# Kernel tuning notes

Measured on AMD Instinct MI355X. Metric: run time of the kernel, lower is better.

Reference implementation:

```python
import jax, jax.numpy as jnp
import numpy as np
from jax import lax

B, T, H, E, N, K = 1024, 64, 512, 200000, 50000, 2
LN_EPS = 1e-5


def _layernorm(x, w, b):
    m = jnp.mean(x, axis=-1, keepdims=True)
    v = jnp.mean((x - m) ** 2, axis=-1, keepdims=True)
    return (x - m) * lax.rsqrt(v + LN_EPS) * w + b


def setup_inputs() -> dict:
    key = jax.random.key(0)
    ks = jax.random.split(key, 12)
    s = 1.0 / np.sqrt(H)
    actions = jax.random.randint(ks[0], (B, T), 0, E, dtype=jnp.int32)
    # each graph stops at a random step in [T//2, T]; actions after that are -1 (stop)
    stop_len = jax.random.randint(ks[1], (B,), T // 2, T + 1, dtype=jnp.int32)
    actions = jnp.where(jnp.arange(T)[None, :] >= stop_len[:, None], -1, actions)
    return {
        "actions_seq": actions,
        "edge_tokens": jax.random.normal(ks[2], (E, H), dtype=jnp.float32),
        "stop_indices": jnp.full((B,), E, dtype=jnp.int32),  # never equals a real edge id
        "question_tokens": jax.random.normal(ks[3], (B, H), dtype=jnp.float32),
        "node_tokens": jax.random.normal(ks[4], (N, H), dtype=jnp.float32),
        "start_node_locals": jax.random.randint(ks[5], (B * K,), 0, N, dtype=jnp.int32),
        "start_ptr": (jnp.arange(B + 1, dtype=jnp.int32) * K),
        "w_ih": jax.random.normal(ks[6], (3 * H, H), dtype=jnp.float32) * s,
        "w_hh": jax.random.normal(ks[7], (3 * H, H), dtype=jnp.float32) * s,
        "b_ih": jax.random.normal(ks[8], (3 * H,), dtype=jnp.float32) * s,
        "b_hh": jax.random.normal(ks[9], (3 * H,), dtype=jnp.float32) * s,
        "ln_w": jnp.ones((H,), dtype=jnp.float32),
        "ln_b": jnp.zeros((H,), dtype=jnp.float32),
    }


def reference(actions_seq, edge_tokens, stop_indices, question_tokens, node_tokens,
              start_node_locals, start_ptr, w_ih, w_hh, b_ih, b_hh, ln_w, ln_b):
    num_graphs, num_steps = actions_seq.shape
    max_edge = edge_tokens.shape[0]

    # start state: segment-mean of selected node tokens per graph
    counts = start_ptr[1:] - start_ptr[:-1]  # [B]
    seg = jnp.repeat(jnp.arange(num_graphs), counts,
                     total_repeat_length=start_node_locals.shape[0])
    start_sum = jax.ops.segment_sum(node_tokens[start_node_locals], seg,
                                    num_segments=num_graphs)  # [B,H]
    denom = jnp.maximum(counts, 1).astype(start_sum.dtype)[:, None]
    start_state = start_sum / denom

    h0 = _layernorm(question_tokens + start_state, ln_w, ln_b)
    done0 = jnp.zeros((num_graphs,), dtype=bool)

    def step(carry, a):  # a: [B] actions at this step
        h, done = carry
        emb = _layernorm(h, ln_w, ln_b)  # emitted BEFORE the update, as in torch
        is_stop = (a == stop_indices) | (a < 0)
        active = (~done) & (~is_stop)
        idx = jnp.clip(a, 0, max_edge - 1)
        x = edge_tokens[idx]  # [B,H] gather (dropout p=0 -> identity)
        gi = x @ w_ih.T + b_ih  # [B,3H]
        gh = h @ w_hh.T + b_hh  # [B,3H]
        i_r, i_z, i_n = jnp.split(gi, 3, axis=-1)
        h_r, h_z, h_n = jnp.split(gh, 3, axis=-1)
        r = jax.nn.sigmoid(i_r + h_r)
        z = jax.nn.sigmoid(i_z + h_z)
        n = jnp.tanh(i_n + r * h_n)
        h_next = (1.0 - z) * n + z * h
        h = jnp.where(active[:, None], h_next, h)
        done = done | is_stop
        return (h, done), emb

    (_, _), embs = lax.scan(step, (h0, done0), actions_seq.T)  # embs: [T,B,H]
    return jnp.transpose(embs, (1, 0, 2))  # [B,T,H]
```

## Files before the change

kernel.cpp:

```cpp
#include <hip/hip_runtime.h>
#include <math.h>

#define NB 1024
#define NT 64
#define NH 512
#define NE 200000
#define LN_EPS 1e-5f

typedef __bf16 bf16;
typedef __attribute__((ext_vector_type(8))) __bf16 bf16x8;
typedef __attribute__((ext_vector_type(4))) float f32x4;

__device__ __forceinline__ void ln_stats(float sum, float sq, float& mean, float& rstd) {
#pragma unroll
  for (int o = 32; o > 0; o >>= 1) {
    sum += __shfl_down(sum, o);
    sq  += __shfl_down(sq, o);
  }
  __shared__ float red[8];
  const int wid = threadIdx.x >> 6;
  if ((threadIdx.x & 63) == 0) { red[wid * 2] = sum; red[wid * 2 + 1] = sq; }
  __syncthreads();
  if (threadIdx.x == 0) {
    const float ts = red[0] + red[2] + red[4] + red[6];
    const float tq = red[1] + red[3] + red[5] + red[7];
    const float m  = ts * (1.0f / NH);
    const float var = tq * (1.0f / NH) - m * m;
    red[0] = m;
    red[1] = rsqrtf(var + LN_EPS);
  }
  __syncthreads();
  mean = red[0];
  rstd = red[1];
}

__device__ __forceinline__ float sigmoid_f(float x) {
  return 1.0f / (1.0f + __expf(-x));
}
__device__ __forceinline__ float tanh_f(float x) {
  x = fminf(fmaxf(x, -15.0f), 15.0f);
  const float e = __expf(2.0f * x);
  return (e - 1.0f) / (e + 1.0f);
}

__global__ void active_kernel(const int* __restrict__ actions,
                              const int* __restrict__ stopidx,
                              int* __restrict__ act_mask) {
  const int b = blockIdx.x * blockDim.x + threadIdx.x;
  if (b >= NB) return;
  const int si = stopidx[b];
  bool done = false;
  for (int t = 0; t < NT; ++t) {
    const int a = actions[b * NT + t];
    const bool is_stop = (a == si) || (a < 0);
    act_mask[b * NT + t] = (!done && !is_stop) ? 1 : 0;
    done = done || is_stop;
  }
}

__global__ void wcvt_kernel(const float* __restrict__ wih,
                            const float* __restrict__ whh,
                            bf16* __restrict__ wihb, bf16* __restrict__ whhb) {
  const int i = (blockIdx.x * 256 + threadIdx.x) * 4;
  const float4 a = *(const float4*)&wih[i];
  const float4 b = *(const float4*)&whh[i];
  union { bf16 h[4]; uint2 u; } pa, pb;
  pa.h[0] = (bf16)a.x; pa.h[1] = (bf16)a.y; pa.h[2] = (bf16)a.z; pa.h[3] = (bf16)a.w;
  pb.h[0] = (bf16)b.x; pb.h[1] = (bf16)b.y; pb.h[2] = (bf16)b.z; pb.h[3] = (bf16)b.w;
  *(uint2*)&wihb[i] = pa.u;
  *(uint2*)&whhb[i] = pb.u;
}

__global__ void xall_kernel(const int* __restrict__ actions,
                            const float* __restrict__ edges,
                            bf16* __restrict__ xbf) {
  const int row = blockIdx.x;
  int a = actions[row];
  a = min(max(a, 0), NE - 1);
  const int i = threadIdx.x * 2;
  const float2 v = *(const float2*)&edges[(size_t)a * NH + i];
  union { bf16 h[2]; unsigned u; } p;
  p.h[0] = (bf16)v.x; p.h[1] = (bf16)v.y;
  *(unsigned*)&xbf[(size_t)row * NH + i] = p.u;
}

__global__ void h0_kernel(const float* __restrict__ q,
                          const float* __restrict__ nodes,
                          const int* __restrict__ locals,
                          const int* __restrict__ ptr,
                          const float* __restrict__ lnw,
                          const float* __restrict__ lnb,
                          float* __restrict__ h0, bf16* __restrict__ h0b) {
  const int b = blockIdx.x;
  const int i = threadIdx.x * 2;
  const int p0 = ptr[b], p1 = ptr[b + 1];
  const float denom = fmaxf((float)(p1 - p0), 1.0f);
  float s0 = 0.f, s1 = 0.f;
  for (int p = p0; p < p1; ++p) {
    const int node = locals[p];
    const float2 nv = *(const float2*)&nodes[(size_t)node * NH + i];
    s0 += nv.x; s1 += nv.y;
  }
  const float2 qv = *(const float2*)&q[(size_t)b * NH + i];
  const float v0 = qv.x + s0 / denom;
  const float v1 = qv.y + s1 / denom;
  float mean, rstd;
  ln_stats(v0 + v1, v0 * v0 + v1 * v1, mean, rstd);
  const float2 lw = *(const float2*)&lnw[i];
  const float2 lb = *(const float2*)&lnb[i];
  float2 o;
  o.x = (v0 - mean) * rstd * lw.x + lb.x;
  o.y = (v1 - mean) * rstd * lw.y + lb.y;
  *(float2*)&h0[(size_t)b * NH + i] = o;
  union { bf16 h[2]; unsigned u; } p;
  p.h[0] = (bf16)o.x; p.h[1] = (bf16)o.y;
  *(unsigned*)&h0b[(size_t)b * NH + i] = p.u;
}

#define BK 128
__global__ __launch_bounds__(512) void gates_kernel(
    const float* __restrict__ hs_t, float* __restrict__ hs_n,
    const bf16* __restrict__ hbf, bf16* __restrict__ hbf_n,
    const bf16* __restrict__ xbf,
    const bf16* __restrict__ wihb, const bf16* __restrict__ whhb,
    const float* __restrict__ b_ih, const float* __restrict__ b_hh,
    const int* __restrict__ act_mask, int t) {
  __shared__ bf16 Xs[64][BK + 8];
  __shared__ bf16 Hs[64][BK + 8];
  __shared__ bf16 Wi[96][BK + 8];
  __shared__ bf16 Wh[96][BK + 8];
  __shared__ int s_any;

  const int tid = threadIdx.x;
  const int c0 = blockIdx.x * 32;
  const int b0 = blockIdx.y * 64;

  if (tid == 0) s_any = 0;
  __syncthreads();
  if (tid < 64 && act_mask[(b0 + tid) * NT + t]) s_any = 1;
  __syncthreads();

  if (!s_any) {
    const int row = tid >> 3, c4 = (tid & 7) * 4;
    const size_t off = (size_t)(b0 + row) * NH + c0 + c4;
    const float4 v = *(const float4*)&hs_t[off];
    *(float4*)&hs_n[off] = v;
    union { bf16 h[4]; uint2 u; } p;
    p.h[0] = (bf16)v.x; p.h[1] = (bf16)v.y; p.h[2] = (bf16)v.z; p.h[3] = (bf16)v.w;
    *(uint2*)&hbf_n[off] = p.u;
    return;
  }

  const int wave = tid >> 6, lane = tid & 63;
  const int ln15 = lane & 15, q8 = (lane >> 4) * 8;
  const int wrow = (wave & 3) * 16;
  const int nt = wave >> 2;

  f32x4 aR = {0, 0, 0, 0}, aZ = {0, 0, 0, 0}, aNI = {0, 0, 0, 0}, aNH = {0, 0, 0, 0};

  for (int kb = 0; kb < NH; kb += BK) {
    if (kb) __syncthreads();
#pragma unroll
    for (int i = 0; i < 2; ++i) {
      const int idx = tid + 512 * i;
      const int row = idx >> 4, c8 = (idx & 15) * 8;
      *(int4*)&Hs[row][c8] = *(const int4*)&hbf[(size_t)(b0 + row) * NH + kb + c8];
      *(int4*)&Xs[row][c8] =
          *(const int4*)&xbf[((size_t)(b0 + row) * NT + t) * NH + kb + c8];
    }
#pragma unroll
    for (int i = 0; i < 3; ++i) {
      const int idx = tid + 512 * i;
      const int row = idx >> 4, c8 = (idx & 15) * 8;
      const int g = row >> 5, n = row & 31;
      const size_t gr = ((size_t)g * NH + c0 + n) * NH + kb + c8;
      *(int4*)&Wi[row][c8] = *(const int4*)&wihb[gr];
      *(int4*)&Wh[row][c8] = *(const int4*)&whhb[gr];
    }
    __syncthreads();
#pragma unroll
    for (int k = 0; k < BK; k += 32) {
      const bf16x8 ax = *(const bf16x8*)&Xs[wrow + ln15][k + q8];
      const bf16x8 ah = *(const bf16x8*)&Hs[wrow + ln15][k + q8];
      const int wr = nt * 16 + ln15;
      const bf16x8 biR = *(const bf16x8*)&Wi[wr][k + q8];
      const bf16x8 bhR = *(const bf16x8*)&Wh[wr][k + q8];
      const bf16x8 biZ = *(const bf16x8*)&Wi[32 + wr][k + q8];
      const bf16x8 bhZ = *(const bf16x8*)&Wh[32 + wr][k + q8];
      const bf16x8 biN = *(const bf16x8*)&Wi[64 + wr][k + q8];
      const bf16x8 bhN = *(const bf16x8*)&Wh[64 + wr][k + q8];
      aR = __builtin_amdgcn_mfma_f32_16x16x32_bf16(ax, biR, aR, 0, 0, 0);
      aR = __builtin_amdgcn_mfma_f32_16x16x32_bf16(ah, bhR, aR, 0, 0, 0);
      aZ = __builtin_amdgcn_mfma_f32_16x16x32_bf16(ax, biZ, aZ, 0, 0, 0);
      aZ = __builtin_amdgcn_mfma_f32_16x16x32_bf16(ah, bhZ, aZ, 0, 0, 0);
      aNI = __builtin_amdgcn_mfma_f32_16x16x32_bf16(ax, biN, aNI, 0, 0, 0);
      aNH = __builtin_amdgcn_mfma_f32_16x16x32_bf16(ah, bhN, aNH, 0, 0, 0);
    }
  }

  const int c = c0 + nt * 16 + ln15;
  const float bR = b_ih[c] + b_hh[c];
  const float bZ = b_ih[NH + c] + b_hh[NH + c];
  const float bI = b_ih[2 * NH + c];
  const float bH = b_hh[2 * NH + c];
  const int mbase = b0 + wrow + (lane >> 4) * 4;
#pragma unroll
  for (int i = 0; i < 4; ++i) {
    const int m = mbase + i;
    const int act = act_mask[m * NT + t];
    const float hp = hs_t[(size_t)m * NH + c];
    const float r = sigmoid_f(aR[i] + bR);
    const float z = sigmoid_f(aZ[i] + bZ);
    const float n = tanh_f(aNI[i] + bI + r * (aNH[i] + bH));
    const float o = act ? ((1.0f - z) * n + z * hp) : hp;
    hs_n[(size_t)m * NH + c] = o;
    hbf_n[(size_t)m * NH + c] = (bf16)o;
  }
}

__global__ void ln_all_kernel(const float* __restrict__ hs,
                              const float* __restrict__ lnw,
                              const float* __restrict__ lnb,
                              float* __restrict__ out) {
  const int r = blockIdx.x;
  const int t = r >> 10, b = r & (NB - 1);
  const int i = threadIdx.x * 2;
  const float2 hv = *(const float2*)&hs[(size_t)r * NH + i];
  float mean, rstd;
  ln_stats(hv.x + hv.y, hv.x * hv.x + hv.y * hv.y, mean, rstd);
  const float2 lw = *(const float2*)&lnw[i];
  const float2 lb = *(const float2*)&lnb[i];
  float2 o;
  o.x = (hv.x - mean) * rstd * lw.x + lb.x;
  o.y = (hv.y - mean) * rstd * lw.y + lb.y;
  *(float2*)&out[((size_t)b * NT + t) * NH + i] = o;
}

extern "C" void kernel_launch(void* const* d_in, const int* in_sizes, int n_in,
                              void* d_out, int out_size, void* d_ws, size_t ws_size,
                              hipStream_t stream) {
  const int*   actions      = (const int*)d_in[0];
  const float* edge_tokens  = (const float*)d_in[1];
  const int*   stop_indices = (const int*)d_in[2];
  const float* question     = (const float*)d_in[3];
  const float* node_tokens  = (const float*)d_in[4];
  const int*   start_locals = (const int*)d_in[5];
  const int*   start_ptr    = (const int*)d_in[6];
  const float* w_ih         = (const float*)d_in[7];
  const float* w_hh         = (const float*)d_in[8];
  const float* b_ih         = (const float*)d_in[9];
  const float* b_hh         = (const float*)d_in[10];
  const float* ln_w         = (const float*)d_in[11];
  const float* ln_b         = (const float*)d_in[12];
  float* out = (float*)d_out;

  bf16* Wihbf = (bf16*)d_ws;
  bf16* Whhbf = Wihbf + (size_t)3 * NH * NH;
  bf16* Xbf   = Whhbf + (size_t)3 * NH * NH;
  float* hstates = (float*)(Xbf + (size_t)NB * NT * NH);
  bf16* Hb0 = (bf16*)(hstates + (size_t)NT * NB * NH);
  bf16* Hb1 = Hb0 + (size_t)NB * NH;
  int* act_mask = (int*)(Hb1 + (size_t)NB * NH);

  active_kernel<<<NB / 256, 256, 0, stream>>>(actions, stop_indices, act_mask);
  wcvt_kernel<<<(3 * NH * NH) / (256 * 4), 256, 0, stream>>>(w_ih, w_hh, Wihbf, Whhbf);
  xall_kernel<<<NB * NT, 256, 0, stream>>>(actions, edge_tokens, Xbf);
  h0_kernel<<<NB, 256, 0, stream>>>(question, node_tokens, start_locals, start_ptr,
                                    ln_w, ln_b, hstates, Hb0);

  bf16* hbc = Hb0;
  bf16* hbn = Hb1;
  for (int t = 0; t < NT - 1; ++t) {
    gates_kernel<<<dim3(NH / 32, NB / 64), 512, 0, stream>>>(
        hstates + (size_t)t * NB * NH, hstates + (size_t)(t + 1) * NB * NH,
        hbc, hbn, Xbf, Wihbf, Whhbf, b_ih, b_hh, act_mask, t);
    bf16* tmp = hbc; hbc = hbn; hbn = tmp;
  }

  ln_all_kernel<<<NB * NT, 256, 0, stream>>>(hstates, ln_w, ln_b, out);
}
```

Before: 1.401 ms.

## Fuse recurrent steps into persistent cooperative kernel with weights resident in LDS

Replaces the 63 per-step gate kernel launches with one cooperative persistent kernel of 256 blocks. Each block keeps its slice of both weight matrices in LDS for the whole run, and the blocks of one batch tile are synchronised through a global atomic counter barrier. The K dimension is split across two wave groups and reduced through LDS, and the mask and x buffers are stored time-major for coalesced access. This removes launch overhead and repeated weight reloads, but drops the skip for fully inactive tiles, adds spin-wait barrier cost, and relies on a guard timeout that could silently break the barrier.

New measurement: 2.271 ms. 62.1% more time.

```diff
diff --git a/kernel.cpp b/kernel.cpp
--- a/kernel.cpp
+++ b/kernel.cpp
@@ -45,7 +45,7 @@
 
 __global__ void active_kernel(const int* __restrict__ actions,
                               const int* __restrict__ stopidx,
-                              int* __restrict__ act_mask) {
+                              int* __restrict__ mask_T) {
   const int b = blockIdx.x * blockDim.x + threadIdx.x;
   if (b >= NB) return;
   const int si = stopidx[b];
@@ -53,7 +53,7 @@
   for (int t = 0; t < NT; ++t) {
     const int a = actions[b * NT + t];
     const bool is_stop = (a == si) || (a < 0);
-    act_mask[b * NT + t] = (!done && !is_stop) ? 1 : 0;
+    mask_T[t * NB + b] = (!done && !is_stop) ? 1 : 0;
     done = done || is_stop;
   }
 }
@@ -74,14 +74,15 @@
 __global__ void xall_kernel(const int* __restrict__ actions,
                             const float* __restrict__ edges,
                             bf16* __restrict__ xbf) {
-  const int row = blockIdx.x;
-  int a = actions[row];
+  const int blk = blockIdx.x;
+  const int b = blk >> 6, t = blk & 63;
+  int a = actions[blk];
   a = min(max(a, 0), NE - 1);
   const int i = threadIdx.x * 2;
   const float2 v = *(const float2*)&edges[(size_t)a * NH + i];
   union { bf16 h[2]; unsigned u; } p;
   p.h[0] = (bf16)v.x; p.h[1] = (bf16)v.y;
-  *(unsigned*)&xbf[(size_t)row * NH + i] = p.u;
+  *(unsigned*)&xbf[((size_t)t * NB + b) * NH + i] = p.u;
 }
 
 __global__ void h0_kernel(const float* __restrict__ q,
@@ -117,104 +118,149 @@
   *(unsigned*)&h0b[(size_t)b * NH + i] = p.u;
 }
 
-#define BK 128
-__global__ __launch_bounds__(512) void gates_kernel(
-    const float* __restrict__ hs_t, float* __restrict__ hs_n,
-    const bf16* __restrict__ hbf, bf16* __restrict__ hbf_n,
+#define MFMA_BF16 __builtin_amdgcn_mfma_f32_16x16x32_bf16
+__global__ __launch_bounds__(512, 2) void pers_kernel(
+    float* __restrict__ hstates,
+    bf16* __restrict__ hbf0, bf16* __restrict__ hbf1,
     const bf16* __restrict__ xbf,
     const bf16* __restrict__ wihb, const bf16* __restrict__ whhb,
     const float* __restrict__ b_ih, const float* __restrict__ b_hh,
-    const int* __restrict__ act_mask, int t) {
-  __shared__ bf16 Xs[64][BK + 8];
-  __shared__ bf16 Hs[64][BK + 8];
-  __shared__ bf16 Wi[96][BK + 8];
-  __shared__ bf16 Wh[96][BK + 8];
-  __shared__ int s_any;
+    const int* __restrict__ mask_T,
+    int* __restrict__ cnt) {
+  __shared__ bf16 Wi[48][520];
+  __shared__ bf16 Wh[48][520];
+  __shared__ float red[8][4][64][4];
 
   const int tid = threadIdx.x;
-  const int c0 = blockIdx.x * 32;
-  const int b0 = blockIdx.y * 64;
-
-  if (tid == 0) s_any = 0;
+  const int blk = blockIdx.x;
+  const int btile = blk & 7;
+  const int ctile = blk >> 3;
+  const int b0 = btile * 128;
+  const int c0 = ctile * 16;
+
+  for (int i = tid; i < 48 * 64; i += 512) {
+    const int row = i >> 6, ch = (i & 63) * 8;
+    const int g = row >> 4, n = row & 15;
+    const size_t src = ((size_t)(g * NH + c0 + n)) * NH + ch;
+    *(int4*)&Wi[row][ch] = *(const int4*)&wihb[src];
+    *(int4*)&Wh[row][ch] = *(const int4*)&whhb[src];
+  }
   __syncthreads();
-  if (tid < 64 && act_mask[(b0 + tid) * NT + t]) s_any = 1;
-  __syncthreads();
-
-  if (!s_any) {
-    const int row = tid >> 3, c4 = (tid & 7) * 4;
-    const size_t off = (size_t)(b0 + row) * NH + c0 + c4;
-    const float4 v = *(const float4*)&hs_t[off];
-    *(float4*)&hs_n[off] = v;
-    union { bf16 h[4]; uint2 u; } p;
-    p.h[0] = (bf16)v.x; p.h[1] = (bf16)v.y; p.h[2] = (bf16)v.z; p.h[3] = (bf16)v.w;
-    *(uint2*)&hbf_n[off] = p.u;
-    return;
-  }
 
   const int wave = tid >> 6, lane = tid & 63;
   const int ln15 = lane & 15, q8 = (lane >> 4) * 8;
-  const int wrow = (wave & 3) * 16;
-  const int nt = wave >> 2;
-
-  f32x4 aR = {0, 0, 0, 0}, aZ = {0, 0, 0, 0}, aNI = {0, 0, 0, 0}, aNH = {0, 0, 0, 0};
-
-  for (int kb = 0; kb < NH; kb += BK) {
-    if (kb) __syncthreads();
-#pragma unroll
-    for (int i = 0; i < 2; ++i) {
-      const int idx = tid + 512 * i;
-      const int row = idx >> 4, c8 = (idx & 15) * 8;
-      *(int4*)&Hs[row][c8] = *(const int4*)&hbf[(size_t)(b0 + row) * NH + kb + c8];
-      *(int4*)&Xs[row][c8] =
-          *(const int4*)&xbf[((size_t)(b0 + row) * NT + t) * NH + kb + c8];
-    }
-#pragma unroll
-    for (int i = 0; i < 3; ++i) {
-      const int idx = tid + 512 * i;
-      const int row = idx >> 4, c8 = (idx & 15) * 8;
-      const int g = row >> 5, n = row & 31;
-      const size_t gr = ((size_t)g * NH + c0 + n) * NH + kb + c8;
-      *(int4*)&Wi[row][c8] = *(const int4*)&wihb[gr];
-      *(int4*)&Wh[row][c8] = *(const int4*)&whhb[gr];
-    }
-    __syncthreads();
-#pragma unroll
-    for (int k = 0; k < BK; k += 32) {
-      const bf16x8 ax = *(const bf16x8*)&Xs[wrow + ln15][k + q8];
-      const bf16x8 ah = *(const bf16x8*)&Hs[wrow + ln15][k + q8];
-      const int wr = nt * 16 + ln15;
-      const bf16x8 biR = *(const bf16x8*)&Wi[wr][k + q8];
-      const bf16x8 bhR = *(const bf16x8*)&Wh[wr][k + q8];
-      const bf16x8 biZ = *(const bf16x8*)&Wi[32 + wr][k + q8];
-      const bf16x8 bhZ = *(const bf16x8*)&Wh[32 + wr][k + q8];
-      const bf16x8 biN = *(const bf16x8*)&Wi[64 + wr][k + q8];
-      const bf16x8 bhN = *(const bf16x8*)&Wh[64 + wr][k + q8];
-      aR = __builtin_amdgcn_mfma_f32_16x16x32_bf16(ax, biR, aR, 0, 0, 0);
-      aR = __builtin_amdgcn_mfma_f32_16x16x32_bf16(ah, bhR, aR, 0, 0, 0);
-      aZ = __builtin_amdgcn_mfma_f32_16x16x32_bf16(ax, biZ, aZ, 0, 0, 0);
-      aZ = __builtin_amdgcn_mfma_f32_16x16x32_bf16(ah, bhZ, aZ, 0, 0, 0);
-      aNI = __builtin_amdgcn_mfma_f32_16x16x32_bf16(ax, biN, aNI, 0, 0, 0);
-      aNH = __builtin_amdgcn_mfma_f32_16x16x32_bf16(ah, bhN, aNH, 0, 0, 0);
-    }
-  }
-
-  const int c = c0 + nt * 16 + ln15;
+  const int mw = wave & 3, kw = wave >> 2;
+  const int mbase = b0 + mw * 32;
+  const int k0 = kw * 256;
+
+  const int c = c0 + ln15;
   const float bR = b_ih[c] + b_hh[c];
   const float bZ = b_ih[NH + c] + b_hh[NH + c];
   const float bI = b_ih[2 * NH + c];
   const float bH = b_hh[2 * NH + c];
-  const int mbase = b0 + wrow + (lane >> 4) * 4;
+
+  const bf16* hb_cur = hbf0;
+  bf16* hb_nxt = hbf1;
+
+  for (int t = 0; t < NT - 1; ++t) {
+    const bf16* xrow0 = &xbf[((size_t)t * NB + mbase + ln15) * NH + k0 + q8];
+    const bf16* xrow1 = xrow0 + 16 * NH;
+    const bf16* hrow0 = &hb_cur[(size_t)(mbase + ln15) * NH + k0 + q8];
+    const bf16* hrow1 = hrow0 + 16 * NH;
+
+    f32x4 aR0 = {0,0,0,0}, aR1 = {0,0,0,0}, aZ0 = {0,0,0,0}, aZ1 = {0,0,0,0};
+    f32x4 aNI0 = {0,0,0,0}, aNI1 = {0,0,0,0}, aNH0 = {0,0,0,0}, aNH1 = {0,0,0,0};
 #pragma unroll
-  for (int i = 0; i < 4; ++i) {
-    const int m = mbase + i;
-    const int act = act_mask[m * NT + t];
-    const float hp = hs_t[(size_t)m * NH + c];
-    const float r = sigmoid_f(aR[i] + bR);
-    const float z = sigmoid_f(aZ[i] + bZ);
-    const float n = tanh_f(aNI[i] + bI + r * (aNH[i] + bH));
-    const float o = act ? ((1.0f - z) * n + z * hp) : hp;
-    hs_n[(size_t)m * NH + c] = o;
-    hbf_n[(size_t)m * NH + c] = (bf16)o;
+    for (int kc = 0; kc < 256; kc += 32) {
+      const bf16x8 ax0 = *(const bf16x8*)(xrow0 + kc);
+      const bf16x8 ax1 = *(const bf16x8*)(xrow1 + kc);
+      const bf16x8 ah0 = *(const bf16x8*)(hrow0 + kc);
+      const bf16x8 ah1 = *(const bf16x8*)(hrow1 + kc);
+      const int kk = k0 + kc + q8;
+      const bf16x8 biR = *(const bf16x8*)&Wi[ln15][kk];
+      const bf16x8 bhR = *(const bf16x8*)&Wh[ln15][kk];
+      const bf16x8 biZ = *(const bf16x8*)&Wi[16 + ln15][kk];
+      const bf16x8 bhZ = *(const bf16x8*)&Wh[16 + ln15][kk];
+      const bf16x8 biN = *(const bf16x8*)&Wi[32 + ln15][kk];
+      const bf16x8 bhN = *(const bf16x8*)&Wh[32 + ln15][kk];
+      aR0 = MFMA_BF16(ax0, biR, aR0, 0, 0, 0);
+      aR1 = MFMA_BF16(ax1, biR, aR1, 0, 0, 0);
+      aZ0 = MFMA_BF16(ax0, biZ, aZ0, 0, 0, 0);
+      aZ1 = MFMA_BF16(ax1, biZ, aZ1, 0, 0, 0);
+      aNI0 = MFMA_BF16(ax0, biN, aNI0, 0, 0, 0);
+      aNI1 = MFMA_BF16(ax1, biN, aNI1, 0, 0, 0);
+      aR0 = MFMA_BF16(ah0, bhR, aR0, 0, 0, 0);
+      aR1 = MFMA_BF16(ah1, bhR, aR1, 0, 0, 0);
+      aZ0 = MFMA_BF16(ah0, bhZ, aZ0, 0, 0, 0);
+      aZ1 = MFMA_BF16(ah1, bhZ, aZ1, 0, 0, 0);
+      aNH0 = MFMA_BF16(ah0, bhN, aNH0, 0, 0, 0);
+      aNH1 = MFMA_BF16(ah1, bhN, aNH1, 0, 0, 0);
+    }
+
+    if (kw == 1) {
+      *(f32x4*)&red[0][mw][lane][0] = aR0;
+      *(f32x4*)&red[1][mw][lane][0] = aR1;
+      *(f32x4*)&red[2][mw][lane][0] = aZ0;
+      *(f32x4*)&red[3][mw][lane][0] = aZ1;
+      *(f32x4*)&red[4][mw][lane][0] = aNI0;
+      *(f32x4*)&red[5][mw][lane][0] = aNI1;
+      *(f32x4*)&red[6][mw][lane][0] = aNH0;
+      *(f32x4*)&red[7][mw][lane][0] = aNH1;
+    }
+    __syncthreads();
+    if (kw == 0) {
+      aR0 += *(const f32x4*)&red[0][mw][lane][0];
+      aR1 += *(const f32x4*)&red[1][mw][lane][0];
+      aZ0 += *(const f32x4*)&red[2][mw][lane][0];
+      aZ1 += *(const f32x4*)&red[3][mw][lane][0];
+      aNI0 += *(const f32x4*)&red[4][mw][lane][0];
+      aNI1 += *(const f32x4*)&red[5][mw][lane][0];
+      aNH0 += *(const f32x4*)&red[6][mw][lane][0];
+      aNH1 += *(const f32x4*)&red[7][mw][lane][0];
+
+      const int r4 = (lane >> 4) * 4;
+#pragma unroll
+      for (int sub = 0; sub < 2; ++sub) {
+        const f32x4 vR = sub ? aR1 : aR0;
+        const f32x4 vZ = sub ? aZ1 : aZ0;
+        const f32x4 vNI = sub ? aNI1 : aNI0;
+        const f32x4 vNH = sub ? aNH1 : aNH0;
+        const int ms = mbase + sub * 16 + r4;
+        const int4 mk = *(const int4*)&mask_T[t * NB + ms];
+        const int mks[4] = {mk.x, mk.y, mk.z, mk.w};
+#pragma unroll
+        for (int i = 0; i < 4; ++i) {
+          const int m = ms + i;
+          const float hp = hstates[((size_t)t * NB + m) * NH + c];
+          const float r = sigmoid_f(vR[i] + bR);
+          const float z = sigmoid_f(vZ[i] + bZ);
+          const float n = tanh_f(vNI[i] + bI + r * (vNH[i] + bH));
+          const float o = mks[i] ? ((1.0f - z) * n + z * hp) : hp;
+          hstates[((size_t)(t + 1) * NB + m) * NH + c] = o;
+          hb_nxt[(size_t)m * NH + c] = (bf16)o;
+        }
+      }
+    }
+
+    __syncthreads();
+    if (t < NT - 2) {
+      if (tid == 0) {
+        __threadfence();
+        atomicAdd(&cnt[btile], 1);
+        const int target = 32 * (t + 1);
+        int guard = 0;
+        while (__hip_atomic_load(&cnt[btile], __ATOMIC_RELAXED,
+                                 __HIP_MEMORY_SCOPE_AGENT) < target) {
+          __builtin_amdgcn_s_sleep(2);
+          if (++guard > (1 << 22)) break;
+        }
+        __threadfence();
+      }
+      __syncthreads();
+      __threadfence_block();
+    }
+
+    const bf16* tmp = hb_cur; hb_cur = hb_nxt; hb_nxt = (bf16*)tmp;
   }
 }
 
@@ -260,22 +306,21 @@
   float* hstates = (float*)(Xbf + (size_t)NB * NT * NH);
   bf16* Hb0 = (bf16*)(hstates + (size_t)NT * NB * NH);
   bf16* Hb1 = Hb0 + (size_t)NB * NH;
-  int* act_mask = (int*)(Hb1 + (size_t)NB * NH);
-
-  active_kernel<<<NB / 256, 256, 0, stream>>>(actions, stop_indices, act_mask);
+  int* mask_T = (int*)(Hb1 + (size_t)NB * NH);
+  int* cnt = mask_T + NT * NB;
+
+  hipMemsetAsync(cnt, 0, 8 * sizeof(int), stream);
+  active_kernel<<<NB / 256, 256, 0, stream>>>(actions, stop_indices, mask_T);
   wcvt_kernel<<<(3 * NH * NH) / (256 * 4), 256, 0, stream>>>(w_ih, w_hh, Wihbf, Whhbf);
   xall_kernel<<<NB * NT, 256, 0, stream>>>(actions, edge_tokens, Xbf);
   h0_kernel<<<NB, 256, 0, stream>>>(question, node_tokens, start_locals, start_ptr,
                                     ln_w, ln_b, hstates, Hb0);
 
-  bf16* hbc = Hb0;
-  bf16* hbn = Hb1;
-  for (int t = 0; t < NT - 1; ++t) {
-    gates_kernel<<<dim3(NH / 32, NB / 64), 512, 0, stream>>>(
-        hstates + (size_t)t * NB * NH, hstates + (size_t)(t + 1) * NB * NH,
-        hbc, hbn, Xbf, Wihbf, Whhbf, b_ih, b_hh, act_mask, t);
-    bf16* tmp = hbc; hbc = hbn; hbn = tmp;
-  }
+  void* kargs[] = {(void*)&hstates, (void*)&Hb0, (void*)&Hb1, (void*)&Xbf,
+                   (void*)&Wihbf, (void*)&Whhbf, (void*)&b_ih, (void*)&b_hh,
+                   (void*)&mask_T, (void*)&cnt};
+  hipLaunchCooperativeKernel((const void*)pers_kernel, dim3(256), dim3(512),
+                             kargs, 0, stream);
 
   ln_all_kernel<<<NB * NT, 256, 0, stream>>>(hstates, ln_w, ln_b, out);
 }
```
